# Performance work log

Measured on AMD Instinct MI355X. Metric: run time of the kernel, lower is better.

## Reference

```python
import jax, jax.numpy as jnp
import numpy as np

B, T, I, H = 4096, 2048, 4, 3


def setup_inputs() -> dict:
    key = jax.random.key(0)
    ks = jax.random.split(key, 6)
    input_seq = jax.random.normal(ks[0], (B, T, I), dtype=jnp.float32)
    # pack_padded_sequence(enforce_sorted=True) requires descending lengths; max == T
    length = jnp.sort(jax.random.randint(ks[1], (B,), 1, T + 1))[::-1]
    length = length.at[0].set(T).astype(jnp.int64)
    s = 0.1
    W_ih = jax.random.normal(ks[2], (4 * H, I), dtype=jnp.float32) * s  # gate order: i,f,g,o
    W_hh = jax.random.normal(ks[3], (4 * H, H), dtype=jnp.float32) * s
    b_ih = jax.random.normal(ks[4], (4 * H,), dtype=jnp.float32) * s
    b_hh = jax.random.normal(ks[5], (4 * H,), dtype=jnp.float32) * s
    return {"input_seq": input_seq, "W_ih": W_ih, "W_hh": W_hh,
            "b_ih": b_ih, "b_hh": b_hh, "length": length}


def _lstm_padded(input_seq, W_ih, W_hh, b_ih, b_hh, length):
    # Precompute input projections for all timesteps: [B,T,4H]
    x_proj = jnp.einsum('bti,gi->btg', input_seq, W_ih) + (b_ih + b_hh)
    x_proj_t = jnp.swapaxes(x_proj, 0, 1)  # [T,B,4H]

    def step(carry, xg):
        h, c = carry
        gates = xg + h @ W_hh.T  # [B,4H]
        i, f, g, o = jnp.split(gates, 4, axis=-1)
        i = jax.nn.sigmoid(i)
        f = jax.nn.sigmoid(f)
        g = jnp.tanh(g)
        o = jax.nn.sigmoid(o)
        c = f * c + i * g
        h = o * jnp.tanh(c)
        return (h, c), h

    h0 = jnp.zeros((B, H), dtype=input_seq.dtype)
    c0 = jnp.zeros((B, H), dtype=input_seq.dtype)
    _, hs = jax.lax.scan(step, (h0, c0), x_proj_t)  # hs: [T,B,H]
    hs = jnp.swapaxes(hs, 0, 1)  # [B,T,H]
    # pad_packed_sequence zeros out positions t >= length; valid prefix is unaffected
    mask = (jnp.arange(T)[None, :] < length[:, None])[..., None]
    return jnp.where(mask, hs, 0.0)


def reference(input_seq, W_ih, W_hh, b_ih, b_hh, length):
    return _lstm_padded(input_seq, W_ih, W_hh, b_ih, b_hh, length)
```

## Files before the change

### kernel.cpp

```cpp
#include <hip/hip_runtime.h>


#define BB 4096
#define TT 2048
#define L2E 1.4426950408889634f

template<int CTRL>
__device__ __forceinline__ float dppf(float v) {
    return __int_as_float(
        __builtin_amdgcn_update_dpp(0, __float_as_int(v), CTRL, 0xF, 0xF, true));
}

__global__ __launch_bounds__(64, 1) void lstm_seq(
    const float* __restrict__ x, const float* __restrict__ Wih,
    const float* __restrict__ Whh, const float* __restrict__ bih,
    const float* __restrict__ bhh, const int* __restrict__ len,
    float* __restrict__ out)
{
    const int lane  = threadIdx.x & 63;
    const int s     = lane & 3;
    const int q     = (lane >> 2) & 3;
    const int row16 = lane >> 4;
    const int b     = blockIdx.x * 4 + row16;
    const int u     = (q < 3) ? q : 2;
    const int wrow  = s * 3 + u;

    const float scale = (s == 2) ? (2.f * L2E) : (-L2E);
    const float Aa = (s == 2) ? (2.f * L2E) : 0.f;
    const float Bb = (s == 2) ? (-4.f * L2E) : 1.f;

    const float xw0 = Wih[wrow * 4 + 0] * scale;
    const float xw1 = Wih[wrow * 4 + 1] * scale;
    const float xw2 = Wih[wrow * 4 + 2] * scale;
    const float xw3 = Wih[wrow * 4 + 3] * scale;
    const float bias = (bih[wrow] + bhh[wrow]) * scale;

    float wh[4];
    #pragma unroll
    for (int j = 0; j < 4; ++j) {
        const int srcq = (q - j) & 3;
        wh[j] = (srcq == 3) ? 0.f : Whh[wrow * 3 + srcq] * scale;
    }

    const int mylen = len[b];
    int wmax = mylen;
    #pragma unroll
    for (int off = 1; off < 64; off <<= 1)
        wmax = max(wmax, __shfl_xor(wmax, off));
    const int Tloop = (wmax + 7) & ~7;

    float myh = 0.f, cc = 0.f;
    const float4* __restrict__ xrow = ((const float4*)x) + (size_t)b * TT;
    float* __restrict__ orow = out + (size_t)b * (TT * 3);
    const bool writer = (s == 0) && (q < 3);

    float4 buf[8];
    float xacc[8];
    #pragma unroll
    for (int uu = 0; uu < 8; ++uu) buf[uu] = xrow[uu];

    for (int tb = 0; tb < Tloop; tb += 8) {
        #pragma unroll
        for (int uu = 0; uu < 8; ++uu) {
            const float4 xv = buf[uu];
            xacc[uu] = fmaf(xw3, xv.w, fmaf(xw2, xv.z,
                       fmaf(xw1, xv.y, fmaf(xw0, xv.x, bias))));
        }
        #pragma unroll
        for (int uu = 0; uu < 8; ++uu) {
            const int tn = tb + 8 + uu;
            buf[uu] = xrow[tn < TT ? tn : 0];
        }
        #pragma unroll
        for (int uu = 0; uu < 8; ++uu) {
            const int t = tb + uu;
            const float hs1 = dppf<0x124>(myh);
            const float hs2 = dppf<0x128>(myh);
            const float hs3 = dppf<0x12C>(myh);
            const float a = fmaf(wh[3], hs3, fmaf(wh[2], hs2,
                            fmaf(wh[1], hs1, fmaf(wh[0], myh, xacc[uu]))));
            const float r = __builtin_amdgcn_rcpf(1.f + __builtin_amdgcn_exp2f(a));
            const float act = fmaf(Bb, r, Aa);
            const float gi = dppf<0x00>(act);
            const float gf = dppf<0x55>(act);
            const float gg = dppf<0xAA>(act);
            const float go = dppf<0xFF>(act);
            cc = fmaf(gf, cc, gi * gg);
            const float tcv = fmaf(-2.f,
                __builtin_amdgcn_rcpf(1.f + __builtin_amdgcn_exp2f(cc)), 1.f);
            myh = go * tcv;
            if (writer) orow[t * 3 + q] = (t < mylen) ? myh : 0.f;
        }
    }

    const int start4 = Tloop * 3 / 4;
    #pragma unroll
    for (int rr = 0; rr < 4; ++rr) {
        float4* __restrict__ o4 = (float4*)(out + ((size_t)(blockIdx.x * 4 + rr)) * (TT * 3));
        for (int idx = start4 + lane; idx < TT * 3 / 4; idx += 64)
            o4[idx] = make_float4(0.f, 0.f, 0.f, 0.f);
    }
}

extern "C" void kernel_launch(void* const* d_in, const int* in_sizes, int n_in,
                              void* d_out, int out_size, void* d_ws, size_t ws_size,
                              hipStream_t stream) {
    const float* x    = (const float*)d_in[0];
    const float* Wih  = (const float*)d_in[1];
    const float* Whh  = (const float*)d_in[2];
    const float* bih  = (const float*)d_in[3];
    const float* bhh  = (const float*)d_in[4];
    const int*   lenp = (const int*)d_in[5];
    float* out = (float*)d_out;

    lstm_seq<<<BB / 4, 64, 0, stream>>>(x, Wih, Whh, bih, bhh, lenp, out);
}
```

Measured before the change: 427.8 us.

## Remap lanes so each lane computes all four gates for one hidden unit

Lanes are reassigned so that each lane owns one hidden unit of one batch row and computes all four gates itself. Each wave now covers 16 batch rows instead of 4, and the grid shrinks to a quarter of the blocks. This drops the per-step DPP broadcast of gate activations and gives four independent exp/rcp chains per step, aiming to shorten the serial recurrence latency. In exchange each lane does more VALU work per step, and far fewer waves are resident, so fewer SIMDs are used across the GPU.

```diff
diff --git a/kernel.cpp b/kernel.cpp
--- a/kernel.cpp
+++ b/kernel.cpp
@@ -17,29 +17,25 @@
     const float* __restrict__ bhh, const int* __restrict__ len,
     float* __restrict__ out)
 {
-    const int lane  = threadIdx.x & 63;
-    const int s     = lane & 3;
-    const int q     = (lane >> 2) & 3;
-    const int row16 = lane >> 4;
-    const int b     = blockIdx.x * 4 + row16;
-    const int u     = (q < 3) ? q : 2;
-    const int wrow  = s * 3 + u;
+    const int lane = threadIdx.x & 63;
+    const int u    = lane & 3;
+    const int j    = lane >> 2;
+    const int b    = blockIdx.x * 16 + j;
+    const int ur   = (u < 3) ? u : 2;
 
-    const float scale = (s == 2) ? (2.f * L2E) : (-L2E);
-    const float Aa = (s == 2) ? (2.f * L2E) : 0.f;
-    const float Bb = (s == 2) ? (-4.f * L2E) : 1.f;
-
-    const float xw0 = Wih[wrow * 4 + 0] * scale;
-    const float xw1 = Wih[wrow * 4 + 1] * scale;
-    const float xw2 = Wih[wrow * 4 + 2] * scale;
-    const float xw3 = Wih[wrow * 4 + 3] * scale;
-    const float bias = (bih[wrow] + bhh[wrow]) * scale;
-
-    float wh[4];
+    float xw[4][4], bias[4], wh[4][4];
     #pragma unroll
-    for (int j = 0; j < 4; ++j) {
-        const int srcq = (q - j) & 3;
-        wh[j] = (srcq == 3) ? 0.f : Whh[wrow * 3 + srcq] * scale;
+    for (int g = 0; g < 4; ++g) {
+        const float sc = (g == 2) ? (2.f * L2E) : (-L2E);
+        const int r = g * 3 + ur;
+        #pragma unroll
+        for (int k = 0; k < 4; ++k) xw[g][k] = Wih[r * 4 + k] * sc;
+        bias[g] = (bih[r] + bhh[r]) * sc;
+        #pragma unroll
+        for (int k = 0; k < 4; ++k) {
+            const int su = (u + k) & 3;
+            wh[g][k] = (su == 3) ? 0.f : Whh[r * 3 + su] * sc;
+        }
     }
 
     const int mylen = len[b];
@@ -52,51 +48,61 @@
     float myh = 0.f, cc = 0.f;
     const float4* __restrict__ xrow = ((const float4*)x) + (size_t)b * TT;
     float* __restrict__ orow = out + (size_t)b * (TT * 3);
-    const bool writer = (s == 0) && (q < 3);
+    const bool writer = (u < 3);
 
     float4 buf[8];
-    float xacc[8];
+    float4 xa[8];
     #pragma unroll
-    for (int uu = 0; uu < 8; ++uu) buf[uu] = xrow[uu];
+    for (int t0 = 0; t0 < 8; ++t0) buf[t0] = xrow[t0];
 
     for (int tb = 0; tb < Tloop; tb += 8) {
         #pragma unroll
-        for (int uu = 0; uu < 8; ++uu) {
-            const float4 xv = buf[uu];
-            xacc[uu] = fmaf(xw3, xv.w, fmaf(xw2, xv.z,
-                       fmaf(xw1, xv.y, fmaf(xw0, xv.x, bias))));
+        for (int t0 = 0; t0 < 8; ++t0) {
+            const float4 xv = buf[t0];
+            xa[t0].x = fmaf(xw[0][3], xv.w, fmaf(xw[0][2], xv.z,
+                       fmaf(xw[0][1], xv.y, fmaf(xw[0][0], xv.x, bias[0]))));
+            xa[t0].y = fmaf(xw[1][3], xv.w, fmaf(xw[1][2], xv.z,
+                       fmaf(xw[1][1], xv.y, fmaf(xw[1][0], xv.x, bias[1]))));
+            xa[t0].z = fmaf(xw[2][3], xv.w, fmaf(xw[2][2], xv.z,
+                       fmaf(xw[2][1], xv.y, fmaf(xw[2][0], xv.x, bias[2]))));
+            xa[t0].w = fmaf(xw[3][3], xv.w, fmaf(xw[3][2], xv.z,
+                       fmaf(xw[3][1], xv.y, fmaf(xw[3][0], xv.x, bias[3]))));
         }
         #pragma unroll
-        for (int uu = 0; uu < 8; ++uu) {
-            const int tn = tb + 8 + uu;
-            buf[uu] = xrow[tn < TT ? tn : 0];
+        for (int t0 = 0; t0 < 8; ++t0) {
+            const int tn = tb + 8 + t0;
+            buf[t0] = xrow[tn < TT ? tn : 0];
         }
         #pragma unroll
-        for (int uu = 0; uu < 8; ++uu) {
-            const int t = tb + uu;
-            const float hs1 = dppf<0x124>(myh);
-            const float hs2 = dppf<0x128>(myh);
-            const float hs3 = dppf<0x12C>(myh);
-            const float a = fmaf(wh[3], hs3, fmaf(wh[2], hs2,
-                            fmaf(wh[1], hs1, fmaf(wh[0], myh, xacc[uu]))));
-            const float r = __builtin_amdgcn_rcpf(1.f + __builtin_amdgcn_exp2f(a));
-            const float act = fmaf(Bb, r, Aa);
-            const float gi = dppf<0x00>(act);
-            const float gf = dppf<0x55>(act);
-            const float gg = dppf<0xAA>(act);
-            const float go = dppf<0xFF>(act);
-            cc = fmaf(gf, cc, gi * gg);
-            const float tcv = fmaf(-2.f,
-                __builtin_amdgcn_rcpf(1.f + __builtin_amdgcn_exp2f(cc)), 1.f);
-            myh = go * tcv;
-            if (writer) orow[t * 3 + q] = (t < mylen) ? myh : 0.f;
+        for (int t0 = 0; t0 < 8; ++t0) {
+            const int t = tb + t0;
+            const float h1 = dppf<0x39>(myh);
+            const float h2 = dppf<0x4E>(myh);
+            const float h3 = dppf<0x93>(myh);
+            float a0 = fmaf(wh[0][0], myh, xa[t0].x);
+            float a1 = fmaf(wh[1][0], myh, xa[t0].y);
+            float a2 = fmaf(wh[2][0], myh, xa[t0].z);
+            float a3 = fmaf(wh[3][0], myh, xa[t0].w);
+            a0 = fmaf(wh[0][3], h3, fmaf(wh[0][2], h2, fmaf(wh[0][1], h1, a0)));
+            a1 = fmaf(wh[1][3], h3, fmaf(wh[1][2], h2, fmaf(wh[1][1], h1, a1)));
+            a2 = fmaf(wh[2][3], h3, fmaf(wh[2][2], h2, fmaf(wh[2][1], h1, a2)));
+            a3 = fmaf(wh[3][3], h3, fmaf(wh[3][2], h2, fmaf(wh[3][1], h1, a3)));
+            const float ri = __builtin_amdgcn_rcpf(1.f + __builtin_amdgcn_exp2f(a0));
+            const float rf = __builtin_amdgcn_rcpf(1.f + __builtin_amdgcn_exp2f(a1));
+            const float rg = __builtin_amdgcn_rcpf(1.f + __builtin_amdgcn_exp2f(a2));
+            const float ro = __builtin_amdgcn_rcpf(1.f + __builtin_amdgcn_exp2f(a3));
+            const float gsc = fmaf(-4.f * L2E, rg, 2.f * L2E);
+            cc = fmaf(rf, cc, ri * gsc);
+            const float r2 = __builtin_amdgcn_rcpf(1.f + __builtin_amdgcn_exp2f(cc));
+            myh = fmaf(-2.f * ro, r2, ro);
+            if (writer) orow[t * 3 + u] = (t < mylen) ? myh : 0.f;
         }
     }
 
     const int start4 = Tloop * 3 / 4;
-    #pragma unroll
-    for (int rr = 0; rr < 4; ++rr) {
-        float4* __restrict__ o4 = (float4*)(out + ((size_t)(blockIdx.x * 4 + rr)) * (TT * 3));
+    for (int rr = 0; rr < 16; ++rr) {
+        float4* __restrict__ o4 =
+            (float4*)(out + ((size_t)(blockIdx.x * 16 + rr)) * (TT * 3));
         for (int idx = start4 + lane; idx < TT * 3 / 4; idx += 64)
             o4[idx] = make_float4(0.f, 0.f, 0.f, 0.f);
     }
@@ -113,5 +119,5 @@
     const int*   lenp = (const int*)d_in[5];
     float* out = (float*)d_out;
 
-    lstm_seq<<<BB / 4, 64, 0, stream>>>(x, Wih, Whh, bih, bhh, lenp, out);
+    lstm_seq<<<BB / 16, 64, 0, stream>>>(x, Wih, Whh, bih, bhh, lenp, out);
 }
```

New measurement: 506.6 us. 1.18x slower.
